# Kernel tuning notes

Measured on AMD Instinct MI355X. Metric: run time of the kernel, lower is better.

The kernel has to match this reference:

```python
import jax, jax.numpy as jnp
import numpy as np

DIM = 1024
DIM_HEAD = 64
HEADS = 16
INNER = DIM_HEAD * HEADS  # 1024
B, N1, N2 = 8, 4096, 256
EPS = 1e-5


def layer_norm(x, w, b):
    mu = jnp.mean(x, axis=-1, keepdims=True)
    var = jnp.var(x, axis=-1, keepdims=True)
    return (x - mu) * jax.lax.rsqrt(var + EPS) * w + b


def setup_inputs() -> dict:
    key = jax.random.key(0)
    ks = jax.random.split(key, 10)
    return {
        "x": jax.random.normal(ks[0], (B, N1, DIM), jnp.float32),
        "latents": jax.random.normal(ks[1], (B, N2, DIM), jnp.float32),
        "shift": jax.random.normal(ks[2], (B, DIM), jnp.float32),
        "scale": jax.random.normal(ks[3], (B, DIM), jnp.float32),
        "ln1_w": jnp.ones((DIM,), jnp.float32),
        "ln1_b": jnp.zeros((DIM,), jnp.float32),
        "ln2_w": jnp.ones((DIM,), jnp.float32),
        "ln2_b": jnp.zeros((DIM,), jnp.float32),
        "Wq": jax.random.normal(ks[4], (INNER, DIM), jnp.float32) * 0.02,
        "Wkv": jax.random.normal(ks[5], (2 * INNER, DIM), jnp.float32) * 0.02,
        "Wo": jax.random.normal(ks[6], (DIM, INNER), jnp.float32) * 0.02,
    }


def reference(x, latents, shift, scale, ln1_w, ln1_b, ln2_w, ln2_b, Wq, Wkv, Wo):
    x = layer_norm(x, ln1_w, ln1_b)                      # (b, n1, D)
    lat = layer_norm(latents, ln2_w, ln2_b)              # (b, n2, D)
    lat = lat * (1.0 + scale[:, None, :]) + shift[:, None, :]

    b, n2, _ = lat.shape
    q = jnp.einsum('bld,ed->ble', lat, Wq)               # (b, n2, inner)
    kv_in = jnp.concatenate((x, lat), axis=-2)           # (b, n1+n2, D)
    kv = jnp.einsum('bld,ed->ble', kv_in, Wkv)           # (b, n1+n2, 2*inner)
    k, v = jnp.split(kv, 2, axis=-1)

    def to_heads(t):
        bsz, L, _ = t.shape
        return t.reshape(bsz, L, HEADS, DIM_HEAD).transpose(0, 2, 1, 3)

    q, k, v = to_heads(q), to_heads(k), to_heads(v)      # (b, h, L, dh)
    attn_scale = 1.0 / np.sqrt(np.sqrt(DIM_HEAD)).astype(np.float32)
    logits = jnp.einsum('bhqd,bhkd->bhqk', q * attn_scale, k * attn_scale)
    w = jax.nn.softmax(logits.astype(jnp.float32), axis=-1).astype(logits.dtype)
    out = jnp.einsum('bhqk,bhkd->bhqd', w, v)            # (b, h, n2, dh)
    out = out.transpose(0, 2, 1, 3).reshape(b, n2, INNER)
    return jnp.einsum('ble,de->bld', out, Wo)            # (b, n2, D)
```

## Files before the change

### kernel.cpp

```cpp
#include <hip/hip_runtime.h>
#include <cstdint>
#include <cstddef>

#define B_SZ 8
#define N1 4096
#define N2 256
#define LTOT 4352
#define DIMD 1024
#define HEADS 16
#define DH 64
#define MKV (B_SZ * LTOT)
#define ATILE 64
#define AITERS (LTOT / ATILE)
#define G0B 1088

typedef _Float16 f16;
typedef f16 f16x4_t __attribute__((ext_vector_type(4)));
typedef f16 f16x8_t __attribute__((ext_vector_type(8)));
typedef float f32x4_t __attribute__((ext_vector_type(4)));

__device__ __forceinline__ void g2l16(const void* g, void* l) {
  __builtin_amdgcn_global_load_lds(
      (__attribute__((address_space(1))) void*)g,
      (__attribute__((address_space(3))) void*)l, 16, 0, 0);
}

__global__ __launch_bounds__(256) void prep_kernel(
    const float* __restrict__ x, const float* __restrict__ lat,
    const float* __restrict__ shift, const float* __restrict__ scale,
    const float* __restrict__ ln1w, const float* __restrict__ ln1b,
    const float* __restrict__ ln2w, const float* __restrict__ ln2b,
    const float* __restrict__ Wq, const float* __restrict__ Wkv,
    const float* __restrict__ Wo, f16* __restrict__ kv_in,
    f16* __restrict__ Wq16, f16* __restrict__ Wkv16, f16* __restrict__ Wo16) {
  const int bid = blockIdx.x;
  const int tid = threadIdx.x;
  if (bid >= MKV) {
    const int c = bid - MKV;
    const float* src;
    f16* dst;
    int off;
    if (c < 1024) { src = Wq; dst = Wq16; off = c; }
    else if (c < 3072) { src = Wkv; dst = Wkv16; off = c - 1024; }
    else { src = Wo; dst = Wo16; off = c - 3072; }
    const int i = off * 256 + tid;
    float4 v = ((const float4*)src)[i];
    f16x4_t o = {(f16)v.x, (f16)v.y, (f16)v.z, (f16)v.w};
    ((f16x4_t*)dst)[i] = o;
    return;
  }
  const int row = bid;
  const int b = row / LTOT;
  const int n = row - b * LTOT;
  const bool is_lat = (n >= N1);
  const float* src = is_lat ? (lat + (size_t)(b * N2 + (n - N1)) * DIMD)
                            : (x + (size_t)(b * N1 + n) * DIMD);
  float4 v = ((const float4*)src)[tid];
  float s = v.x + v.y + v.z + v.w;
  float s2 = v.x * v.x + v.y * v.y + v.z * v.z + v.w * v.w;
#pragma unroll
  for (int m = 1; m <= 32; m <<= 1) {
    s += __shfl_xor(s, m, 64);
    s2 += __shfl_xor(s2, m, 64);
  }
  __shared__ float red[8];
  const int wave = tid >> 6;
  if ((tid & 63) == 0) { red[wave * 2] = s; red[wave * 2 + 1] = s2; }
  __syncthreads();
  s = red[0] + red[2] + red[4] + red[6];
  s2 = red[1] + red[3] + red[5] + red[7];
  const float mean = s * (1.0f / DIMD);
  const float var = fmaxf(s2 * (1.0f / DIMD) - mean * mean, 0.0f);
  const float rstd = rsqrtf(var + 1e-5f);
  const float4 w4 = ((const float4*)(is_lat ? ln2w : ln1w))[tid];
  const float4 b4 = ((const float4*)(is_lat ? ln2b : ln1b))[tid];
  float y0 = (v.x - mean) * rstd * w4.x + b4.x;
  float y1 = (v.y - mean) * rstd * w4.y + b4.y;
  float y2 = (v.z - mean) * rstd * w4.z + b4.z;
  float y3 = (v.w - mean) * rstd * w4.w + b4.w;
  if (is_lat) {
    float4 sc = ((const float4*)(scale + (size_t)b * DIMD))[tid];
    float4 sh = ((const float4*)(shift + (size_t)b * DIMD))[tid];
    y0 = y0 * (1.0f + sc.x) + sh.x;
    y1 = y1 * (1.0f + sc.y) + sh.y;
    y2 = y2 * (1.0f + sc.z) + sh.z;
    y3 = y3 * (1.0f + sc.w) + sh.w;
  }
  f16x4_t o = {(f16)y0, (f16)y1, (f16)y2, (f16)y3};
  *(f16x4_t*)(kv_in + (size_t)row * DIMD + tid * 4) = o;
}

#define DS_A(buf, mh)                                                          \
  _Pragma("unroll") for (int i_ = 0; i_ < 4; i_++)                             \
  _Pragma("unroll") for (int ks_ = 0; ks_ < 2; ks_++)                          \
      aF[i_][ks_] = *(const f16x8_t*)&As[buf][mh][                             \
          (wrow * 64 + i_ * 16 + r16) * 64 + (((ks_ * 4 + g8i) ^ xk) * 8)];

#define DS_B(dst, buf, nh)                                                     \
  _Pragma("unroll") for (int j_ = 0; j_ < 2; j_++)                             \
  _Pragma("unroll") for (int ks_ = 0; ks_ < 2; ks_++)                          \
      dst[j_][ks_] = *(const f16x8_t*)&Bs[buf][nh][                            \
          (wcol * 32 + j_ * 16 + r16) * 64 + (((ks_ * 4 + g8i) ^ xk) * 8)];

#define MFMA16(mh, nh, BF)                                                     \
  __builtin_amdgcn_s_setprio(1);                                               \
  _Pragma("unroll") for (int ks_ = 0; ks_ < 2; ks_++)                          \
  _Pragma("unroll") for (int i_ = 0; i_ < 4; i_++)                             \
  _Pragma("unroll") for (int j_ = 0; j_ < 2; j_++)                             \
      acc[(mh)*4 + i_][(nh)*2 + j_] = __builtin_amdgcn_mfma_f32_16x16x32_f16(  \
          aF[i_][ks_], BF[j_][ks_], acc[(mh)*4 + i_][(nh)*2 + j_], 0, 0, 0);   \
  __builtin_amdgcn_s_setprio(0);

#define BARR asm volatile("s_barrier" ::: "memory")
#define LGKM0 asm volatile("s_waitcnt lgkmcnt(0)" ::: "memory")
#define VM4 asm volatile("s_waitcnt vmcnt(4)" ::: "memory")

__global__ __launch_bounds__(512, 2) void gemm_pre(
    const f16* __restrict__ kv_in, const f16* __restrict__ Wkv16,
    const f16* __restrict__ Wq16, f16* __restrict__ kbuf,
    f16* __restrict__ vbuf, f16* __restrict__ qbuf) {
  const int id = blockIdx.x;
  const bool is_kv = (id < G0B);
  int mt = 0, nt;
  const f16 *Abase, *Bbase;
  if (is_kv) {
    const int xcd = id & 7, l = id >> 3;
    mt = xcd * 17 + (l >> 3);
    nt = l & 7;
    Abase = kv_in + (size_t)mt * 256 * DIMD;
    Bbase = Wkv16 + (size_t)nt * 256 * DIMD;
  } else {
    const int id2 = id - G0B;
    const int bq = id2 >> 2;
    nt = id2 & 3;
    Abase = kv_in + ((size_t)(bq * LTOT + N1)) * DIMD;
    Bbase = Wq16 + (size_t)nt * 256 * DIMD;
  }
  __shared__ alignas(16) f16 As[2][2][128 * 64];
  __shared__ alignas(16) f16 Bs[2][2][128 * 64];
  const int tid = threadIdx.x;
  const int wave = tid >> 6, lane = tid & 63;
  const int wrow = wave >> 2, wcol = wave & 3;
  const int r16 = lane & 15, g8i = lane >> 4, q4 = (lane >> 4) * 4;
  const int xk = r16 & 7;
  const int t8 = tid >> 3, c8 = tid & 7;
  f32x4_t acc[8][4] = {};
  f16x8_t aF[4][2], b0F[2][2], b1F[2][2];

  const int col8 = (c8 ^ (t8 & 7)) * 8;
  const f16* Asrc = Abase + (size_t)t8 * DIMD + col8;
  const f16* Bsrc = Bbase + (size_t)((t8 >> 5) * 64 + (t8 & 31)) * DIMD + col8;

  auto stageA = [&](int kt, int buf, int mh) {
#pragma unroll
    for (int j = 0; j < 2; j++)
      g2l16(Asrc + (size_t)(j * 128 + mh * 64) * DIMD + kt * 64,
            &As[buf][mh][(j * 512 + wave * 64) * 8]);
  };
  auto stageB = [&](int kt, int buf, int nh) {
#pragma unroll
    for (int j = 0; j < 2; j++)
      g2l16(Bsrc + (size_t)(j * 128 + nh * 32) * DIMD + kt * 64,
            &Bs[buf][nh][(j * 512 + wave * 64) * 8]);
  };

  stageA(0, 0, 0); stageB(0, 0, 1); stageA(0, 0, 1); stageB(0, 0, 0);
  stageA(1, 1, 0); stageB(1, 1, 1);
  VM4; BARR;

#pragma unroll 1
  for (int it = 0; it < 8; ++it) {
    const int kA = 2 * it + 1;
    const int kB = (2 * it + 2 > 15) ? 15 : 2 * it + 2;
    const int kC = (2 * it + 3 > 15) ? 15 : 2 * it + 3;
    DS_A(0, 0); DS_B(b0F, 0, 0);
    stageA(kA, 1, 1);
    BARR; LGKM0; MFMA16(0, 0, b0F);
    DS_B(b1F, 0, 1);
    stageB(kA, 1, 0);
    BARR; LGKM0; MFMA16(0, 1, b1F);
    DS_A(0, 1);
    stageA(kB, 0, 0);
    BARR; LGKM0; MFMA16(1, 1, b1F);
    stageB(kB, 0, 1);
    VM4;
    BARR; LGKM0; MFMA16(1, 0, b0F);
    DS_A(1, 0); DS_B(b0F, 1, 0);
    stageA(kB, 0, 1);
    BARR; LGKM0; MFMA16(0, 0, b0F);
    DS_B(b1F, 1, 1);
    stageB(kB, 0, 0);
    BARR; LGKM0; MFMA16(0, 1, b1F);
    DS_A(1, 1);
    stageA(kC, 1, 0);
    BARR; LGKM0; MFMA16(1, 1, b1F);
    stageB(kC, 1, 1);
    VM4;
    BARR; LGKM0; MFMA16(1, 0, b0F);
  }
  asm volatile("s_waitcnt vmcnt(0)" ::: "memory");

  if (is_kv) {
    const int m0 = mt * 256;
    const int b = m0 / LTOT;
    const int n0 = m0 - b * LTOT;
    if (nt < 4) {
#pragma unroll
      for (int ai = 0; ai < 8; ai++) {
        const int n_base = n0 + wrow * 128 + (ai >> 2) * 64 + (ai & 3) * 16 + q4;
#pragma unroll
        for (int bj = 0; bj < 4; bj++) {
          const int e = nt * 256 + wcol * 64 + (bj >> 1) * 32 + (bj & 1) * 16 + r16;
          const int h = e >> 6, d = e & 63;
          const size_t base = (size_t)(b * HEADS + h) * LTOT;
#pragma unroll
          for (int r = 0; r < 4; r++)
            kbuf[(base + n_base + r) * DH + d] = (f16)acc[ai][bj][r];
        }
      }
    } else {
#pragma unroll
      for (int ai = 0; ai < 8; ai++) {
        const int n_base = n0 + wrow * 128 + (ai >> 2) * 64 + (ai & 3) * 16 + q4;
#pragma unroll
        for (int bj = 0; bj < 4; bj++) {
          const int e = (nt - 4) * 256 + wcol * 64 + (bj >> 1) * 32 + (bj & 1) * 16 + r16;
          const int h = e >> 6, d = e & 63;
          f16x4_t pk = {(f16)acc[ai][bj][0], (f16)acc[ai][bj][1],
                        (f16)acc[ai][bj][2], (f16)acc[ai][bj][3]};
          *(f16x4_t*)&vbuf[((size_t)(b * HEADS + h) * DH + d) * LTOT + n_base] = pk;
        }
      }
    }
  } else {
    const int b = (id - G0B) >> 2;
#pragma unroll
    for (int ai = 0; ai < 8; ai++) {
      const int qn = wrow * 128 + (ai >> 2) * 64 + (ai & 3) * 16 + q4;
#pragma unroll
      for (int bj = 0; bj < 4; bj++) {
        const int e = nt * 256 + wcol * 64 + (bj >> 1) * 32 + (bj & 1) * 16 + r16;
        const int h = e >> 6, d = e & 63;
#pragma unroll
        for (int r = 0; r < 4; r++)
          qbuf[((size_t)(b * HEADS + h) * N2 + qn + r) * DH + d] = (f16)acc[ai][bj][r];
      }
    }
  }
}

__global__ __launch_bounds__(256) void gemm_out(
    const f16* __restrict__ A0, const f16* __restrict__ BT,
    float* __restrict__ outp) {
  const int id = blockIdx.x;
  const int mt = id >> 4, nt = id & 15;
  const f16* Abase = A0 + (size_t)mt * 128 * DIMD;
  const f16* Bbase = BT + (size_t)nt * 64 * DIMD;
  __shared__ alignas(16) f16 As[2][128 * 32];
  __shared__ alignas(16) f16 Bs[2][64 * 32];
  const int tid = threadIdx.x;
  const int wave = tid >> 6, lane = tid & 63;
  const int wm = (wave & 1) * 64, wn = (wave >> 1) * 32;
  const int lrow = lane >> 2;
  const int r16 = lane & 15, q4 = (lane >> 4) * 4;
  const int lcol_sw = (((lane & 3) ^ ((lrow >> 1) & 3)) * 8);
  const int g8sw = (((lane >> 4) ^ ((r16 >> 1) & 3)) * 8);
  f32x4_t acc[4][2] = {};

  auto stage = [&](int k0, int buf) {
    g2l16(Abase + (size_t)(wave * 16 + lrow) * DIMD + k0 + lcol_sw, &As[buf][(wave * 16) * 32]);
    g2l16(Abase + (size_t)(64 + wave * 16 + lrow) * DIMD + k0 + lcol_sw, &As[buf][(64 + wave * 16) * 32]);
    g2l16(Bbase + (size_t)(wave * 16 + lrow) * DIMD + k0 + lcol_sw, &Bs[buf][(wave * 16) * 32]);
  };
  auto body = [&](int kt, int cur) {
    if (kt < 31) asm volatile("s_waitcnt vmcnt(3)" ::: "memory");
    else         asm volatile("s_waitcnt vmcnt(0)" ::: "memory");
    asm volatile("s_barrier" ::: "memory");
    f16x8_t a[4], bf[2];
#pragma unroll
    for (int i = 0; i < 4; i++)
      a[i] = *(const f16x8_t*)&As[cur][(wm + i * 16 + r16) * 32 + g8sw];
#pragma unroll
    for (int j = 0; j < 2; j++)
      bf[j] = *(const f16x8_t*)&Bs[cur][(wn + j * 16 + r16) * 32 + g8sw];
#pragma unroll
    for (int i = 0; i < 4; i++)
#pragma unroll
      for (int j = 0; j < 2; j++)
        acc[i][j] = __builtin_amdgcn_mfma_f32_16x16x32_f16(a[i], bf[j], acc[i][j], 0, 0, 0);
    asm volatile("s_waitcnt lgkmcnt(0)" ::: "memory");
    asm volatile("s_barrier" ::: "memory");
    if (kt + 2 < 32) stage((kt + 2) * 32, cur);
  };
  stage(0, 0);
  stage(32, 1);
#pragma unroll 1
  for (int kt = 0; kt < 32; kt += 2) { body(kt, 0); body(kt + 1, 1); }

  const int m0 = mt * 128, n0 = nt * 64;
#pragma unroll
  for (int i = 0; i < 4; i++) {
#pragma unroll
    for (int j = 0; j < 2; j++) {
      const int col = n0 + wn + j * 16 + r16;
#pragma unroll
      for (int r = 0; r < 4; r++)
        outp[(size_t)(m0 + wm + i * 16 + q4 + r) * DIMD + col] = acc[i][j][r];
    }
  }
}

__global__ __launch_bounds__(512, 2) void attn_kernel(
    const f16* __restrict__ qbuf, const f16* __restrict__ kbuf,
    const f16* __restrict__ vbuf, f16* __restrict__ attn_out) {
  const int bh = blockIdx.x & 127;
  const int qt = blockIdx.x >> 7;
  const int b = bh >> 4, h = bh & 15;
  const f16* qg = qbuf + ((size_t)bh * N2 + qt * 128) * DH;
  const f16* kg = kbuf + (size_t)bh * LTOT * DH;
  const f16* vg = vbuf + (size_t)bh * DH * LTOT;

  __shared__ alignas(16) f16 Ks[2][4096];
  __shared__ alignas(16) f16 Vs[2][4096];
  __shared__ alignas(16) f16 QP[9216];

  const int tid = threadIdx.x, wave = tid >> 6, lane = tid & 63;
  const int lrow = lane >> 2;
  const int r16 = lane & 15, g8 = (lane >> 4) * 8, q4 = (lane >> 4) * 4;
  const int lcol_sw = (((lane & 3) ^ ((lrow >> 1) & 3)) * 8);
  const int g8sw = (((lane >> 4) ^ ((r16 >> 1) & 3)) * 8);
  f16* Ps = &QP[wave * 1152];

#pragma unroll
  for (int i = 0; i < 2; i++) {
    const int c = wave * 2 + i, s = c >> 3, rb = (c & 7) * 16;
    g2l16(qg + (size_t)(rb + lrow) * DH + s * 32 + lcol_sw, &QP[s * 4096 + rb * 32]);
  }
  auto stage = [&](int kt, int buf) {
    const int s = wave >> 2, rb = (wave & 3) * 16;
    g2l16(kg + (size_t)(kt * ATILE + rb + lrow) * DH + s * 32 + lcol_sw,
          &Ks[buf][s * 2048 + rb * 32]);
    g2l16(vg + (size_t)(rb + lrow) * LTOT + kt * ATILE + s * 32 + lcol_sw,
          &Vs[buf][s * 2048 + rb * 32]);
  };
  stage(0, 0);
  stage(1, 1);
  asm volatile("s_waitcnt vmcnt(4)" ::: "memory");
  asm volatile("s_barrier" ::: "memory");
  f16x8_t bQ[2];
#pragma unroll
  for (int s = 0; s < 2; s++)
    bQ[s] = *(const f16x8_t*)&QP[s * 4096 + (wave * 16 + r16) * 32 + g8sw];
  asm volatile("s_waitcnt lgkmcnt(0)" ::: "memory");

  f32x4_t oacc[4] = {};
  float mrow = -1e30f, lsum = 0.0f;
  const float SCL = 0.125f * 1.44269504089f;

  for (int kt = 0; kt < AITERS; kt++) {
    const int cur = kt & 1;
    asm volatile("s_waitcnt vmcnt(2)" ::: "memory");
    asm volatile("s_barrier" ::: "memory");
    f32x4_t sacc[4] = {};
    __builtin_amdgcn_s_setprio(1);
#pragma unroll
    for (int s = 0; s < 2; s++) {
      f16x8_t aK[4];
#pragma unroll
      for (int i = 0; i < 4; i++)
        aK[i] = *(const f16x8_t*)&Ks[cur][s * 2048 + (i * 16 + r16) * 32 + g8sw];
#pragma unroll
      for (int i = 0; i < 4; i++)
        sacc[i] = __builtin_amdgcn_mfma_f32_16x16x32_f16(aK[i], bQ[s], sacc[i], 0, 0, 0);
    }
    __builtin_amdgcn_s_setprio(0);
    float vmax = -1e30f;
#pragma unroll
    for (int i = 0; i < 4; i++)
#pragma unroll
      for (int r = 0; r < 4; r++) vmax = fmaxf(vmax, sacc[i][r]);
    vmax = fmaxf(vmax, __shfl_xor(vmax, 16, 64));
    vmax = fmaxf(vmax, __shfl_xor(vmax, 32, 64));
    const float pm = SCL * vmax;
    if (!__all(pm <= mrow + 8.0f)) {
      const float m_new = fmaxf(mrow, pm);
      const float alpha = exp2f(mrow - m_new);
      lsum *= alpha;
#pragma unroll
      for (int id = 0; id < 4; id++) oacc[id] *= alpha;
      mrow = m_new;
    }
    float psum = 0.0f;
#pragma unroll
    for (int i = 0; i < 4; i++) {
      f16x4_t pk;
#pragma unroll
      for (int r = 0; r < 4; r++) {
        const float p = exp2f(SCL * sacc[i][r] - mrow);
        psum += p;
        pk[r] = (f16)p;
      }
      *(f16x4_t*)&Ps[r16 * 72 + i * 16 + q4] = pk;
    }
    psum += __shfl_xor(psum, 16, 64);
    psum += __shfl_xor(psum, 32, 64);
    lsum += psum;
    __builtin_amdgcn_s_setprio(1);
#pragma unroll
    for (int s2 = 0; s2 < 2; s2++) {
      f16x8_t aV[4];
#pragma unroll
      for (int id = 0; id < 4; id++)
        aV[id] = *(const f16x8_t*)&Vs[cur][s2 * 2048 + (id * 16 + r16) * 32 + g8sw];
      const f16x8_t bP = *(const f16x8_t*)&Ps[r16 * 72 + s2 * 32 + g8];
#pragma unroll
      for (int id = 0; id < 4; id++)
        oacc[id] = __builtin_amdgcn_mfma_f32_16x16x32_f16(aV[id], bP, oacc[id], 0, 0, 0);
    }
    __builtin_amdgcn_s_setprio(0);
    asm volatile("s_waitcnt lgkmcnt(0)" ::: "memory");
    asm volatile("s_barrier" ::: "memory");
    if (kt + 2 < AITERS) stage(kt + 2, cur);
  }
  const float inv = 1.0f / lsum;
  const int q = qt * 128 + wave * 16 + r16;
  const size_t rowbase = ((size_t)(b * N2 + q)) * DIMD + h * DH;
#pragma unroll
  for (int id = 0; id < 4; id++) {
    f16x4_t pk;
#pragma unroll
    for (int r = 0; r < 4; r++) pk[r] = (f16)(oacc[id][r] * inv);
    *(f16x4_t*)&attn_out[rowbase + id * 16 + q4] = pk;
  }
}

extern "C" void kernel_launch(void* const* d_in, const int* in_sizes, int n_in,
                              void* d_out, int out_size, void* d_ws, size_t ws_size,
                              hipStream_t stream) {
  const float* x     = (const float*)d_in[0];
  const float* lat   = (const float*)d_in[1];
  const float* shift = (const float*)d_in[2];
  const float* scale = (const float*)d_in[3];
  const float* ln1w  = (const float*)d_in[4];
  const float* ln1b  = (const float*)d_in[5];
  const float* ln2w  = (const float*)d_in[6];
  const float* ln2b  = (const float*)d_in[7];
  const float* Wq    = (const float*)d_in[8];
  const float* Wkv   = (const float*)d_in[9];
  const float* Wo    = (const float*)d_in[10];
  float* outp = (float*)d_out;

  char* ws = (char*)d_ws;
  f16* kv_in = (f16*)ws;                 ws += (size_t)MKV * DIMD * 2;
  f16* Wq16  = (f16*)ws;                 ws += (size_t)1024 * 1024 * 2;
  f16* Wkv16 = (f16*)ws;                 ws += (size_t)2048 * 1024 * 2;
  f16* Wo16  = (f16*)ws;                 ws += (size_t)1024 * 1024 * 2;
  f16* qbuf  = (f16*)ws;                 ws += (size_t)B_SZ * HEADS * N2 * DH * 2;
  f16* kbuf  = (f16*)ws;                 ws += (size_t)B_SZ * HEADS * LTOT * DH * 2;
  f16* vbuf  = (f16*)ws;                 ws += (size_t)B_SZ * HEADS * LTOT * DH * 2;
  f16* aout  = (f16*)ws;                 ws += (size_t)B_SZ * N2 * DIMD * 2;

  prep_kernel<<<dim3(MKV + 4096), dim3(256), 0, stream>>>(
      x, lat, shift, scale, ln1w, ln1b, ln2w, ln2b, Wq, Wkv, Wo,
      kv_in, Wq16, Wkv16, Wo16);
  gemm_pre<<<dim3(G0B + 32), dim3(512), 0, stream>>>(
      kv_in, Wkv16, Wq16, kbuf, vbuf, qbuf);
  attn_kernel<<<dim3(256), dim3(512), 0, stream>>>(qbuf, kbuf, vbuf, aout);
  gemm_out<<<dim3(256), dim3(256), 0, stream>>>(aout, Wo16, outp);
}
```

Measured before the change: 518.9 us.

## Shrink attention and output GEMM tiles to double grid size, drop LDS waits

```diff
diff --git a/kernel.cpp b/kernel.cpp
--- a/kernel.cpp
+++ b/kernel.cpp
@@ -112,7 +112,6 @@
   __builtin_amdgcn_s_setprio(0);
 
 #define BARR asm volatile("s_barrier" ::: "memory")
-#define LGKM0 asm volatile("s_waitcnt lgkmcnt(0)" ::: "memory")
 #define VM4 asm volatile("s_waitcnt vmcnt(4)" ::: "memory")
 
 __global__ __launch_bounds__(512, 2) void gemm_pre(
@@ -175,28 +174,28 @@
     const int kC = (2 * it + 3 > 15) ? 15 : 2 * it + 3;
     DS_A(0, 0); DS_B(b0F, 0, 0);
     stageA(kA, 1, 1);
-    BARR; LGKM0; MFMA16(0, 0, b0F);
+    BARR; MFMA16(0, 0, b0F);
     DS_B(b1F, 0, 1);
     stageB(kA, 1, 0);
-    BARR; LGKM0; MFMA16(0, 1, b1F);
+    BARR; MFMA16(0, 1, b1F);
     DS_A(0, 1);
     stageA(kB, 0, 0);
-    BARR; LGKM0; MFMA16(1, 1, b1F);
+    BARR; MFMA16(1, 1, b1F);
     stageB(kB, 0, 1);
     VM4;
-    BARR; LGKM0; MFMA16(1, 0, b0F);
+    BARR; MFMA16(1, 0, b0F);
     DS_A(1, 0); DS_B(b0F, 1, 0);
     stageA(kB, 0, 1);
-    BARR; LGKM0; MFMA16(0, 0, b0F);
+    BARR; MFMA16(0, 0, b0F);
     DS_B(b1F, 1, 1);
     stageB(kB, 0, 0);
-    BARR; LGKM0; MFMA16(0, 1, b1F);
+    BARR; MFMA16(0, 1, b1F);
     DS_A(1, 1);
     stageA(kC, 1, 0);
-    BARR; LGKM0; MFMA16(1, 1, b1F);
+    BARR; MFMA16(1, 1, b1F);
     stageB(kC, 1, 1);
     VM4;
-    BARR; LGKM0; MFMA16(1, 0, b0F);
+    BARR; MFMA16(1, 0, b0F);
   }
   asm volatile("s_waitcnt vmcnt(0)" ::: "memory");
 
@@ -254,75 +253,74 @@
     float* __restrict__ outp) {
   const int id = blockIdx.x;
   const int mt = id >> 4, nt = id & 15;
-  const f16* Abase = A0 + (size_t)mt * 128 * DIMD;
+  const f16* Abase = A0 + (size_t)mt * 64 * DIMD;
   const f16* Bbase = BT + (size_t)nt * 64 * DIMD;
-  __shared__ alignas(16) f16 As[2][128 * 32];
+  __shared__ alignas(16) f16 As[2][64 * 32];
   __shared__ alignas(16) f16 Bs[2][64 * 32];
   const int tid = threadIdx.x;
   const int wave = tid >> 6, lane = tid & 63;
-  const int wm = (wave & 1) * 64, wn = (wave >> 1) * 32;
-  const int lrow = lane >> 2;
+  const int wr = wave >> 1, wc = wave & 1;
   const int r16 = lane & 15, q4 = (lane >> 4) * 4;
-  const int lcol_sw = (((lane & 3) ^ ((lrow >> 1) & 3)) * 8);
   const int g8sw = (((lane >> 4) ^ ((r16 >> 1) & 3)) * 8);
-  f32x4_t acc[4][2] = {};
-
-  auto stage = [&](int k0, int buf) {
-    g2l16(Abase + (size_t)(wave * 16 + lrow) * DIMD + k0 + lcol_sw, &As[buf][(wave * 16) * 32]);
-    g2l16(Abase + (size_t)(64 + wave * 16 + lrow) * DIMD + k0 + lcol_sw, &As[buf][(64 + wave * 16) * 32]);
-    g2l16(Bbase + (size_t)(wave * 16 + lrow) * DIMD + k0 + lcol_sw, &Bs[buf][(wave * 16) * 32]);
+  const int tq = tid >> 2;
+  const int colx = (((tid & 3) ^ ((tq >> 1) & 3)) * 8);
+  const f16* Asrc = Abase + (size_t)tq * DIMD + colx;
+  const f16* Bsrc = Bbase + (size_t)tq * DIMD + colx;
+  f32x4_t acc[2][2] = {};
+
+  auto stage = [&](int kt, int buf) {
+    g2l16(Asrc + kt * 32, &As[buf][wave * 512]);
+    g2l16(Bsrc + kt * 32, &Bs[buf][wave * 512]);
   };
-  auto body = [&](int kt, int cur) {
-    if (kt < 31) asm volatile("s_waitcnt vmcnt(3)" ::: "memory");
-    else         asm volatile("s_waitcnt vmcnt(0)" ::: "memory");
+  stage(0, 0);
+#pragma unroll 1
+  for (int kt = 0; kt < 32; ++kt) {
+    const int cur = kt & 1;
+    stage(kt + 1 < 32 ? kt + 1 : 31, cur ^ 1);
+    asm volatile("s_waitcnt vmcnt(2)" ::: "memory");
     asm volatile("s_barrier" ::: "memory");
-    f16x8_t a[4], bf[2];
-#pragma unroll
-    for (int i = 0; i < 4; i++)
-      a[i] = *(const f16x8_t*)&As[cur][(wm + i * 16 + r16) * 32 + g8sw];
+    f16x8_t a[2], bf[2];
+#pragma unroll
+    for (int i = 0; i < 2; i++)
+      a[i] = *(const f16x8_t*)&As[cur][(wr * 32 + i * 16 + r16) * 32 + g8sw];
 #pragma unroll
     for (int j = 0; j < 2; j++)
-      bf[j] = *(const f16x8_t*)&Bs[cur][(wn + j * 16 + r16) * 32 + g8sw];
-#pragma unroll
-    for (int i = 0; i < 4; i++)
+      bf[j] = *(const f16x8_t*)&Bs[cur][(wc * 32 + j * 16 + r16) * 32 + g8sw];
+#pragma unroll
+    for (int i = 0; i < 2; i++)
 #pragma unroll
       for (int j = 0; j < 2; j++)
         acc[i][j] = __builtin_amdgcn_mfma_f32_16x16x32_f16(a[i], bf[j], acc[i][j], 0, 0, 0);
-    asm volatile("s_waitcnt lgkmcnt(0)" ::: "memory");
     asm volatile("s_barrier" ::: "memory");
-    if (kt + 2 < 32) stage((kt + 2) * 32, cur);
-  };
-  stage(0, 0);
-  stage(32, 1);
-#pragma unroll 1
-  for (int kt = 0; kt < 32; kt += 2) { body(kt, 0); body(kt + 1, 1); }
-
-  const int m0 = mt * 128, n0 = nt * 64;
-#pragma unroll
-  for (int i = 0; i < 4; i++) {
+  }
+  asm volatile("s_waitcnt vmcnt(0)" ::: "memory");
+
+  const int m0 = mt * 64, n0 = nt * 64;
+#pragma unroll
+  for (int i = 0; i < 2; i++) {
 #pragma unroll
     for (int j = 0; j < 2; j++) {
-      const int col = n0 + wn + j * 16 + r16;
+      const int col = n0 + wc * 32 + j * 16 + r16;
 #pragma unroll
       for (int r = 0; r < 4; r++)
-        outp[(size_t)(m0 + wm + i * 16 + q4 + r) * DIMD + col] = acc[i][j][r];
-    }
-  }
-}
-
-__global__ __launch_bounds__(512, 2) void attn_kernel(
+        outp[(size_t)(m0 + wr * 32 + i * 16 + q4 + r) * DIMD + col] = acc[i][j][r];
+    }
+  }
+}
+
+__global__ __launch_bounds__(256, 2) void attn_kernel(
     const f16* __restrict__ qbuf, const f16* __restrict__ kbuf,
     const f16* __restrict__ vbuf, f16* __restrict__ attn_out) {
   const int bh = blockIdx.x & 127;
   const int qt = blockIdx.x >> 7;
   const int b = bh >> 4, h = bh & 15;
-  const f16* qg = qbuf + ((size_t)bh * N2 + qt * 128) * DH;
+  const f16* qg = qbuf + ((size_t)bh * N2 + qt * 64) * DH;
   const f16* kg = kbuf + (size_t)bh * LTOT * DH;
   const f16* vg = vbuf + (size_t)bh * DH * LTOT;
 
   __shared__ alignas(16) f16 Ks[2][4096];
   __shared__ alignas(16) f16 Vs[2][4096];
-  __shared__ alignas(16) f16 QP[9216];
+  __shared__ alignas(16) f16 QP[4608];
 
   const int tid = threadIdx.x, wave = tid >> 6, lane = tid & 63;
   const int lrow = lane >> 2;
@@ -333,24 +331,27 @@
 
 #pragma unroll
   for (int i = 0; i < 2; i++) {
-    const int c = wave * 2 + i, s = c >> 3, rb = (c & 7) * 16;
-    g2l16(qg + (size_t)(rb + lrow) * DH + s * 32 + lcol_sw, &QP[s * 4096 + rb * 32]);
+    const int c = wave * 2 + i, s = c >> 2, rb = (c & 3) * 16;
+    g2l16(qg + (size_t)(rb + lrow) * DH + s * 32 + lcol_sw, &QP[s * 2048 + rb * 32]);
   }
   auto stage = [&](int kt, int buf) {
-    const int s = wave >> 2, rb = (wave & 3) * 16;
-    g2l16(kg + (size_t)(kt * ATILE + rb + lrow) * DH + s * 32 + lcol_sw,
-          &Ks[buf][s * 2048 + rb * 32]);
-    g2l16(vg + (size_t)(rb + lrow) * LTOT + kt * ATILE + s * 32 + lcol_sw,
-          &Vs[buf][s * 2048 + rb * 32]);
+#pragma unroll
+    for (int i = 0; i < 2; i++) {
+      const int c = wave * 2 + i, s = c >> 2, rb = (c & 3) * 16;
+      g2l16(kg + (size_t)(kt * ATILE + rb + lrow) * DH + s * 32 + lcol_sw,
+            &Ks[buf][s * 2048 + rb * 32]);
+      g2l16(vg + (size_t)(rb + lrow) * LTOT + kt * ATILE + s * 32 + lcol_sw,
+            &Vs[buf][s * 2048 + rb * 32]);
+    }
   };
   stage(0, 0);
   stage(1, 1);
-  asm volatile("s_waitcnt vmcnt(4)" ::: "memory");
+  asm volatile("s_waitcnt vmcnt(8)" ::: "memory");
   asm volatile("s_barrier" ::: "memory");
   f16x8_t bQ[2];
 #pragma unroll
   for (int s = 0; s < 2; s++)
-    bQ[s] = *(const f16x8_t*)&QP[s * 4096 + (wave * 16 + r16) * 32 + g8sw];
+    bQ[s] = *(const f16x8_t*)&QP[s * 2048 + (wave * 16 + r16) * 32 + g8sw];
   asm volatile("s_waitcnt lgkmcnt(0)" ::: "memory");
 
   f32x4_t oacc[4] = {};
@@ -359,7 +360,7 @@
 
   for (int kt = 0; kt < AITERS; kt++) {
     const int cur = kt & 1;
-    asm volatile("s_waitcnt vmcnt(2)" ::: "memory");
+    asm volatile("s_waitcnt vmcnt(4)" ::: "memory");
     asm volatile("s_barrier" ::: "memory");
     f32x4_t sacc[4] = {};
     __builtin_amdgcn_s_setprio(1);
@@ -423,7 +424,7 @@
     if (kt + 2 < AITERS) stage(kt + 2, cur);
   }
   const float inv = 1.0f / lsum;
-  const int q = qt * 128 + wave * 16 + r16;
+  const int q = qt * 64 + wave * 16 + r16;
   const size_t rowbase = ((size_t)(b * N2 + q)) * DIMD + h * DH;
 #pragma unroll
   for (int id = 0; id < 4; id++) {
@@ -465,6 +466,6 @@
       kv_in, Wq16, Wkv16, Wo16);
   gemm_pre<<<dim3(G0B + 32), dim3(512), 0, stream>>>(
       kv_in, Wkv16, Wq16, kbuf, vbuf, qbuf);
-  attn_kernel<<<dim3(256), dim3(512), 0, stream>>>(qbuf, kbuf, vbuf, aout);
-  gemm_out<<<dim3(256), dim3(256), 0, stream>>>(aout, Wo16, outp);
-}
+  attn_kernel<<<dim3(512), dim3(256), 0, stream>>>(qbuf, kbuf, vbuf, aout);
+  gemm_out<<<dim3(512), dim3(256), 0, stream>>>(aout, Wo16, outp);
+}
```

Measured after the change: 489.9 us. 5.6% less time.
